# Kernel optimization log

Hardware: AMD Instinct MI355X
Metric: run time of the kernel (lower is better)

Reference implementation:

```python
import jax, jax.numpy as jnp
import numpy as np
from jax import lax

EPS = 1e-5
UPSAMPLE = (256, 256)


def _axis_coords(n_in, n_out, dtype):
    # PyTorch bilinear, align_corners=False: src = (i+0.5)*scale - 0.5, clamped to [0, n_in-1]
    scale = n_in / n_out
    c = jnp.clip((jnp.arange(n_out, dtype=dtype) + 0.5) * scale - 0.5, 0.0, n_in - 1)
    i0 = jnp.floor(c).astype(jnp.int32)
    i1 = jnp.minimum(i0 + 1, n_in - 1)
    w = c - i0.astype(dtype)
    return i0, i1, w


def bilinear_resize(x, out_hw):
    # x: [B, C, H, W] -> [B, C, out_h, out_w]
    B, C, H, W = x.shape
    out_h, out_w = out_hw
    y0, y1, wy = _axis_coords(H, out_h, x.dtype)
    x0, x1, wx = _axis_coords(W, out_w, x.dtype)
    wy = wy[None, None, :, None]
    ry = x[:, :, y0, :] * (1 - wy) + x[:, :, y1, :] * wy  # [B,C,out_h,W]
    out = ry[:, :, :, x0] * (1 - wx) + ry[:, :, :, x1] * wx
    return out


def reference(satellite_feature, drone_feature, gamma, beta):
    b, c, h, w = satellite_feature.shape
    # per-sample cross-correlation via grouped conv: weight [B, C, hk, wk], groups=B
    mm = lax.conv_general_dilated(
        satellite_feature.reshape(1, b * c, h, w),
        drone_feature,
        window_strides=(1, 1),
        padding='VALID',
        feature_group_count=b,
        dimension_numbers=('NCHW', 'OIHW', 'NCHW'),
    )  # [1, B, Ho, Wo]
    mm = jnp.transpose(mm, (1, 0, 2, 3))  # [B, 1, Ho, Wo]
    # BatchNorm2d(1), training mode: batch stats over (B, H, W), biased variance
    mean = jnp.mean(mm, axis=(0, 2, 3), keepdims=True)
    var = jnp.mean((mm - mean) ** 2, axis=(0, 2, 3), keepdims=True)
    mm = (mm - mean) * lax.rsqrt(var + EPS)
    mm = mm * gamma.reshape(1, -1, 1, 1) + beta.reshape(1, -1, 1, 1)
    return bilinear_resize(mm, UPSAMPLE)


def setup_inputs() -> dict:
    key = jax.random.key(0)
    k1, k2 = jax.random.split(key)
    return {
        'satellite_feature': jax.random.normal(k1, (16, 256, 64, 64), dtype=jnp.float32),
        'drone_feature': jax.random.normal(k2, (16, 256, 16, 16), dtype=jnp.float32),
        'gamma': jnp.ones((1,), dtype=jnp.float32),
        'beta': jnp.zeros((1,), dtype=jnp.float32),
    }
```

## Files before the change

kernel.cpp:

```cpp
#include <hip/hip_runtime.h>

using f32x4  = __attribute__((ext_vector_type(4))) float;
using bf16x8 = __attribute__((ext_vector_type(8))) short;

__device__ __forceinline__ unsigned short f2bf(float f) {
    union { float f; unsigned int u; } v; v.f = f;
    unsigned int r = v.u + 0x7fffu + ((v.u >> 16) & 1u);
    return (unsigned short)(r >> 16);
}

__device__ __forceinline__ float bf2f(unsigned short u) {
    union { unsigned int u; float f; } v; v.u = ((unsigned int)u) << 16;
    return v.f;
}

__global__ __launch_bounds__(256) void transposeD_zero(
    const float* __restrict__ x, unsigned short* __restrict__ y, float* __restrict__ mm) {
    __shared__ float tile[32][33];
    int b  = blockIdx.z;
    int p0 = blockIdx.x * 32;
    int c0 = blockIdx.y * 32;
    const float* xb = x + (size_t)b * 256 * 256;
    unsigned short* yb = y + (size_t)b * 256 * 256;
    int tx = threadIdx.x, ty = threadIdx.y;
    #pragma unroll
    for (int i = 0; i < 32; i += 8)
        tile[ty + i][tx] = xb[(size_t)(c0 + ty + i) * 256 + (p0 + tx)];
    __syncthreads();
    int tid = ty * 32 + tx;
    #pragma unroll
    for (int k = 0; k < 2; ++k) {
        int wi = tid * 2 + k;
        int pl = wi >> 4;
        int cp = wi & 15;
        unsigned short lo = f2bf(tile[2 * cp][pl]);
        unsigned short hi = f2bf(tile[2 * cp + 1][pl]);
        unsigned int packed = (unsigned int)lo | ((unsigned int)hi << 16);
        *reinterpret_cast<unsigned int*>(&yb[(size_t)(p0 + pl) * 256 + (c0 + 2 * cp)]) = packed;
    }
    if (blockIdx.z == 0) {
        int bid = blockIdx.y * 8 + blockIdx.x;
        for (int i = bid * 256 + tid; i < 38416; i += 64 * 256) mm[i] = 0.f;
    }
}

__global__ __launch_bounds__(256) void conv_fused(
    const float* __restrict__ S,
    const unsigned short* __restrict__ Dt,
    float* __restrict__ mm) {
    __shared__ __align__(16) char lds[64 * 264 * 2];
    char* base = lds;

    int b = blockIdx.x >> 6;
    int r = blockIdx.x & 63;
    int tid = threadIdx.x;

    {
        int sub = tid & 3;
        int cl  = tid >> 2;
        #pragma unroll
        for (int chunk = 0; chunk < 4; ++chunk) {
            int c = chunk * 64 + cl;
            const float* src = S + (((size_t)(b * 256 + c) * 64 + r) * 64);
            #pragma unroll
            for (int k = 0; k < 4; ++k) {
                int p = 16 * k + 4 * sub;
                f32x4 v = *reinterpret_cast<const f32x4*>(src + p);
                #pragma unroll
                for (int e = 0; e < 4; ++e) {
                    int pe = p + e;
                    int off = pe * 512 + ((((c >> 3) ^ (pe & 15))) << 4) + ((c & 7) << 1);
                    *reinterpret_cast<unsigned short*>(base + off) = f2bf(v[e]);
                }
            }
        }
    }
    __syncthreads();

    int w    = tid >> 6;
    int lane = tid & 63;
    int m    = lane & 15;
    int kg   = lane >> 4;

    const unsigned short* Db = Dt + ((size_t)(b * 256 + 64 * w)) * 256;

    f32x4 acc[4][4];
    #pragma unroll
    for (int i = 0; i < 4; ++i)
        #pragma unroll
        for (int j = 0; j < 4; ++j)
            acc[i][j] = f32x4{0.f, 0.f, 0.f, 0.f};

    #pragma unroll
    for (int step = 0; step < 8; ++step) {
        bf16x8 bfr[4];
        #pragma unroll
        for (int n = 0; n < 4; ++n)
            bfr[n] = *reinterpret_cast<const bf16x8*>(Db + (size_t)(16 * n + m) * 256 + step * 32 + kg * 8);
        bf16x8 af[4];
        #pragma unroll
        for (int pa = 0; pa < 4; ++pa) {
            int p = 16 * pa + m;
            int slot = (4 * step + kg) ^ m;
            af[pa] = *reinterpret_cast<const bf16x8*>(base + p * 512 + slot * 16);
        }
        #pragma unroll
        for (int pa = 0; pa < 4; ++pa)
            #pragma unroll
            for (int n = 0; n < 4; ++n)
                acc[pa][n] = __builtin_amdgcn_mfma_f32_16x16x32_bf16(af[pa], bfr[n], acc[pa][n], 0, 0, 0);
    }

    __syncthreads();

    unsigned short* gt = (unsigned short*)base;
    #pragma unroll
    for (int pa = 0; pa < 4; ++pa)
        #pragma unroll
        for (int n = 0; n < 4; ++n)
            #pragma unroll
            for (int t = 0; t < 4; ++t) {
                int row = 16 * pa + 4 * kg + t;
                int col = 64 * w + 16 * n + m;
                gt[row * 264 + col] = f2bf(acc[pa][n][t]);
            }
    __syncthreads();

    int ilo = (r > 48) ? (r - 48) : 0;
    int ihi = (r < 15) ? r : 15;
    int total = (ihi - ilo + 1) * 49;
    for (int o = tid; o < total; o += 256) {
        int i = ilo + o / 49;
        int x = o % 49;
        int y = r - i;
        float s = 0.f;
        int qb = 16 * i;
        #pragma unroll
        for (int j = 0; j < 16; ++j)
            s += bf2f(gt[(x + j) * 264 + qb + j]);
        atomicAdd(&mm[(size_t)b * 2401 + y * 49 + x], s);
    }
}

__global__ __launch_bounds__(256) void conv_naive(
    const float* __restrict__ S, const float* __restrict__ D, float* __restrict__ mm) {
    int blk = blockIdx.x;
    int b = blk / 2401;
    int yx = blk % 2401;
    int y = yx / 49, x = yx % 49;
    int c = threadIdx.x;
    const float* Sp = S + (((size_t)b * 256 + c) * 64 + y) * 64 + x;
    const float* Dp = D + ((size_t)b * 256 + c) * 256;
    float s = 0.f;
    #pragma unroll
    for (int i = 0; i < 16; ++i)
        #pragma unroll 4
        for (int j = 0; j < 16; ++j)
            s += Sp[i * 64 + j] * Dp[i * 16 + j];
    __shared__ float red[256];
    red[c] = s;
    __syncthreads();
    for (int st = 128; st > 0; st >>= 1) {
        if (c < st) red[c] += red[c + st];
        __syncthreads();
    }
    if (c == 0) mm[blk] = red[0];
}

__global__ __launch_bounds__(1024) void stats_kernel(
    const float* __restrict__ mm, float* __restrict__ stats) {
    __shared__ float ssum[1024];
    __shared__ float ssq[1024];
    int tid = threadIdx.x;
    float s = 0.f, q = 0.f;
    for (int i = tid; i < 38416; i += 1024) {
        float v = mm[i];
        s += v; q += v * v;
    }
    ssum[tid] = s; ssq[tid] = q;
    __syncthreads();
    for (int st = 512; st > 0; st >>= 1) {
        if (tid < st) { ssum[tid] += ssum[tid + st]; ssq[tid] += ssq[tid + st]; }
        __syncthreads();
    }
    if (tid == 0) {
        float mean = ssum[0] / 38416.f;
        float var  = ssq[0] / 38416.f - mean * mean;
        stats[0] = mean;
        stats[1] = rsqrtf(var + 1e-5f);
    }
}

__global__ __launch_bounds__(256) void bilinear_kernel(
    const float* __restrict__ mm, const float* __restrict__ stats,
    const float* __restrict__ gamma, const float* __restrict__ beta,
    float* __restrict__ out) {
    int idx = blockIdx.x * 256 + threadIdx.x;
    int b  = idx >> 16;
    int oy = (idx >> 8) & 255;
    int ox = idx & 255;
    const float scale = 49.0f / 256.0f;
    float cy = fminf(fmaxf((oy + 0.5f) * scale - 0.5f, 0.0f), 48.0f);
    int y0 = (int)cy; int y1 = min(y0 + 1, 48); float wy = cy - (float)y0;
    float cx = fminf(fmaxf((ox + 0.5f) * scale - 0.5f, 0.0f), 48.0f);
    int x0 = (int)cx; int x1 = min(x0 + 1, 48); float wx = cx - (float)x0;
    const float* mb = mm + (size_t)b * 2401;
    float v00 = mb[y0 * 49 + x0];
    float v01 = mb[y0 * 49 + x1];
    float v10 = mb[y1 * 49 + x0];
    float v11 = mb[y1 * 49 + x1];
    float r0 = v00 * (1.f - wy) + v10 * wy;
    float r1 = v01 * (1.f - wy) + v11 * wy;
    float v  = r0 * (1.f - wx) + r1 * wx;
    float mean = stats[0], rstd = stats[1];
    v = (v - mean) * rstd * gamma[0] + beta[0];
    out[idx] = v;
}

extern "C" void kernel_launch(void* const* d_in, const int* in_sizes, int n_in,
                              void* d_out, int out_size, void* d_ws, size_t ws_size,
                              hipStream_t stream) {
    const float* S     = (const float*)d_in[0];
    const float* D     = (const float*)d_in[1];
    const float* gamma = (const float*)d_in[2];
    const float* beta  = (const float*)d_in[3];
    float* out = (float*)d_out;

    char* ws = (char*)d_ws;
    const size_t sizeDt = (size_t)16 * 256 * 256 * 2;
    const size_t sizeMm = (size_t)38416 * 4;
    const size_t offDt = 0;
    const size_t offMm = offDt + sizeDt;
    const size_t offStats = offMm + sizeMm;
    const size_t needFast = offStats + 2 * sizeof(float);

    bool fast = (ws_size >= needFast);
    float* mm;
    float* stats;
    if (fast) {
        mm    = (float*)(ws + offMm);
        stats = (float*)(ws + offStats);
    } else {
        mm    = (float*)ws;
        stats = (float*)(ws + sizeMm);
    }

    if (fast) {
        unsigned short* Dt = (unsigned short*)(ws + offDt);
        transposeD_zero<<<dim3(8, 8, 16), dim3(32, 8), 0, stream>>>(D, Dt, mm);
        conv_fused<<<1024, 256, 0, stream>>>(S, Dt, mm);
    } else {
        conv_naive<<<16 * 2401, 256, 0, stream>>>(S, D, mm);
    }
    stats_kernel<<<1, 1024, 0, stream>>>(mm, stats);
    bilinear_kernel<<<4096, 256, 0, stream>>>(mm, stats, gamma, beta, out);
}
```

Before: 53.20 us.

## Replace atomic accumulation with partial buffer plus separate reduce kernel

```diff
diff --git a/kernel.cpp b/kernel.cpp
--- a/kernel.cpp
+++ b/kernel.cpp
@@ -14,8 +14,8 @@
     return v.f;
 }
 
-__global__ __launch_bounds__(256) void transposeD_zero(
-    const float* __restrict__ x, unsigned short* __restrict__ y, float* __restrict__ mm) {
+__global__ __launch_bounds__(256) void transposeD(
+    const float* __restrict__ x, unsigned short* __restrict__ y) {
     __shared__ float tile[32][33];
     int b  = blockIdx.z;
     int p0 = blockIdx.x * 32;
@@ -38,17 +38,13 @@
         unsigned int packed = (unsigned int)lo | ((unsigned int)hi << 16);
         *reinterpret_cast<unsigned int*>(&yb[(size_t)(p0 + pl) * 256 + (c0 + 2 * cp)]) = packed;
     }
-    if (blockIdx.z == 0) {
-        int bid = blockIdx.y * 8 + blockIdx.x;
-        for (int i = bid * 256 + tid; i < 38416; i += 64 * 256) mm[i] = 0.f;
-    }
-}
-
-__global__ __launch_bounds__(256) void conv_fused(
+}
+
+__global__ __launch_bounds__(256, 4) void conv_fused(
     const float* __restrict__ S,
     const unsigned short* __restrict__ Dt,
-    float* __restrict__ mm) {
-    __shared__ __align__(16) char lds[64 * 264 * 2];
+    float* __restrict__ P) {
+    __shared__ __align__(16) char lds[64 * 262 * 2];
     char* base = lds;
 
     int b = blockIdx.x >> 6;
@@ -58,19 +54,26 @@
     {
         int sub = tid & 3;
         int cl  = tid >> 2;
+        f32x4 v[16];
         #pragma unroll
         for (int chunk = 0; chunk < 4; ++chunk) {
             int c = chunk * 64 + cl;
             const float* src = S + (((size_t)(b * 256 + c) * 64 + r) * 64);
             #pragma unroll
+            for (int k = 0; k < 4; ++k)
+                v[chunk * 4 + k] = *reinterpret_cast<const f32x4*>(src + 16 * k + 4 * sub);
+        }
+        #pragma unroll
+        for (int chunk = 0; chunk < 4; ++chunk) {
+            int c = chunk * 64 + cl;
+            #pragma unroll
             for (int k = 0; k < 4; ++k) {
                 int p = 16 * k + 4 * sub;
-                f32x4 v = *reinterpret_cast<const f32x4*>(src + p);
                 #pragma unroll
                 for (int e = 0; e < 4; ++e) {
                     int pe = p + e;
                     int off = pe * 512 + ((((c >> 3) ^ (pe & 15))) << 4) + ((c & 7) << 1);
-                    *reinterpret_cast<unsigned short*>(base + off) = f2bf(v[e]);
+                    *reinterpret_cast<unsigned short*>(base + off) = f2bf(v[chunk * 4 + k][e]);
                 }
             }
         }
@@ -122,7 +125,7 @@
             for (int t = 0; t < 4; ++t) {
                 int row = 16 * pa + 4 * kg + t;
                 int col = 64 * w + 16 * n + m;
-                gt[row * 264 + col] = f2bf(acc[pa][n][t]);
+                gt[row * 262 + col] = f2bf(acc[pa][n][t]);
             }
     __syncthreads();
 
@@ -132,14 +135,28 @@
     for (int o = tid; o < total; o += 256) {
         int i = ilo + o / 49;
         int x = o % 49;
-        int y = r - i;
         float s = 0.f;
         int qb = 16 * i;
         #pragma unroll
         for (int j = 0; j < 16; ++j)
-            s += bf2f(gt[(x + j) * 264 + qb + j]);
-        atomicAdd(&mm[(size_t)b * 2401 + y * 49 + x], s);
-    }
+            s += bf2f(gt[(x + j) * 262 + qb + j]);
+        P[((size_t)((b * 64 + r) * 16 + i)) * 52 + x] = s;
+    }
+}
+
+__global__ __launch_bounds__(256) void reduce_kernel(
+    const float* __restrict__ P, float* __restrict__ mm) {
+    int idx = blockIdx.x * 256 + threadIdx.x;
+    if (idx >= 38416) return;
+    int b  = idx / 2401;
+    int yx = idx % 2401;
+    int y  = yx / 49;
+    int x  = yx % 49;
+    float s = 0.f;
+    #pragma unroll
+    for (int i = 0; i < 16; ++i)
+        s += P[((size_t)((b * 64 + y + i) * 16 + i)) * 52 + x];
+    mm[idx] = s;
 }
 
 __global__ __launch_bounds__(256) void conv_naive(
@@ -229,10 +246,12 @@
     char* ws = (char*)d_ws;
     const size_t sizeDt = (size_t)16 * 256 * 256 * 2;
     const size_t sizeMm = (size_t)38416 * 4;
+    const size_t sizeP  = (size_t)16 * 64 * 16 * 52 * 4;
     const size_t offDt = 0;
     const size_t offMm = offDt + sizeDt;
     const size_t offStats = offMm + sizeMm;
-    const size_t needFast = offStats + 2 * sizeof(float);
+    const size_t offP = (offStats + 2 * sizeof(float) + 255) & ~(size_t)255;
+    const size_t needFast = offP + sizeP;
 
     bool fast = (ws_size >= needFast);
     float* mm;
@@ -247,8 +266,10 @@
 
     if (fast) {
         unsigned short* Dt = (unsigned short*)(ws + offDt);
-        transposeD_zero<<<dim3(8, 8, 16), dim3(32, 8), 0, stream>>>(D, Dt, mm);
-        conv_fused<<<1024, 256, 0, stream>>>(S, Dt, mm);
+        float* P = (float*)(ws + offP);
+        transposeD<<<dim3(8, 8, 16), dim3(32, 8), 0, stream>>>(D, Dt);
+        conv_fused<<<1024, 256, 0, stream>>>(S, Dt, P);
+        reduce_kernel<<<151, 256, 0, stream>>>(P, mm);
     } else {
         conv_naive<<<16 * 2401, 256, 0, stream>>>(S, D, mm);
     }
```

Result: faster. 52.12 us (-2.0%).
